# Optimization experiments

Hardware: AMD Instinct MI355X
Metric: run time of the kernel (lower is better)

## Reference

```python
import jax, jax.numpy as jnp
import numpy as np

SEQ_LEN = 1024
CHANNELS = 64
UNITS = 32
WIDTH = 64
BATCH = 4
EPS = 1e-7


def setup_inputs() -> dict:
    key = jax.random.key(0)
    ks = jax.random.split(key, 5)
    x = jax.random.normal(ks[0], (BATCH, CHANNELS, SEQ_LEN), dtype=jnp.float32)
    Wt = jax.random.normal(ks[1], (UNITS, CHANNELS), dtype=jnp.float32) * (1.0 / np.sqrt(CHANNELS))
    Wx = jax.random.normal(ks[2], (UNITS, CHANNELS), dtype=jnp.float32) * (1.0 / np.sqrt(CHANNELS))
    Wa_w = jax.random.normal(ks[3], (1, UNITS), dtype=jnp.float32) * (1.0 / np.sqrt(UNITS))
    Wa_b = jnp.zeros((1,), dtype=jnp.float32)
    bh = jnp.zeros((UNITS,), dtype=jnp.float32)
    return {"x": x, "Wt": Wt, "Wx": Wx, "Wa_w": Wa_w, "Wa_b": Wa_b, "bh": bh}


def reference(x, Wt, Wx, Wa_w, Wa_b, bh):
    # x: (B, C, S) -> xt: (B, S, C)
    xt = jnp.transpose(x, (0, 2, 1))
    q = jnp.einsum('bsc,uc->bsu', xt, Wt)          # (B, S, U)
    k = jnp.einsum('bsc,uc->bsu', xt, Wx)          # (B, S, U)
    # additive (Bahdanau) scores: tanh over broadcast sum -> (B, S, S, U)
    h = jnp.tanh(q[:, :, None, :] + k[:, None, :, :] + bh)
    e = jnp.einsum('bstu,u->bst', h, Wa_w[0]) + Wa_b[0]   # (B, S, S)
    e = jnp.exp(e - jnp.max(e, axis=-1, keepdims=True))
    # local window mask: key index t allowed for query s iff s-W//2 <= t < s-W//2+W
    idx = jnp.arange(SEQ_LEN)
    lower = idx - WIDTH // 2                        # (S,)
    mask = (lower[:, None] <= idx[None, :]) & (idx[None, :] < (lower[:, None] + WIDTH))
    e = e * mask.astype(e.dtype)
    a = e / (jnp.sum(e, axis=-1, keepdims=True) + EPS)    # (B, S, S)
    v = jnp.einsum('bst,btc->bsc', a, xt)           # (B, S, C)
    v = jnp.transpose(v, (0, 2, 1))                 # (B, C, S)
    return (v, a)
```

## Files before the change

kernel.cpp:

```cpp
#include <hip/hip_runtime.h>
#include <cstddef>
#include <cmath>

#define SEQ    1024
#define CH     64
#define UNITS  32
#define WIDTH  64
#define HALFW  32
#define BATCH  4
#define EPS    1e-7f

#define TS     8
#define TT     72
#define XS     76
#define SCS    65


__global__ __launch_bounds__(256) void qk_kernel(
    const float* __restrict__ x, const float* __restrict__ Wt,
    const float* __restrict__ Wx, const float* __restrict__ bh,
    float* __restrict__ q2, float* __restrict__ k2)
{
    int bu = blockIdx.x;
    int u  = bu & (UNITS - 1);
    int b  = bu >> 5;
    int s4 = (int)threadIdx.x << 2;

    const float* wt = Wt + u * CH;
    const float* wx = Wx + u * CH;
    const float* xb = x + (size_t)b * CH * SEQ + s4;

    float4 qa = {0.f, 0.f, 0.f, 0.f};
    float4 ka = {0.f, 0.f, 0.f, 0.f};
#pragma unroll
    for (int c = 0; c < CH; ++c) {
        float4 xv = *reinterpret_cast<const float4*>(xb + (size_t)c * SEQ);
        float wtc = wt[c], wxc = wx[c];
        qa.x = fmaf(xv.x, wtc, qa.x); qa.y = fmaf(xv.y, wtc, qa.y);
        qa.z = fmaf(xv.z, wtc, qa.z); qa.w = fmaf(xv.w, wtc, qa.w);
        ka.x = fmaf(xv.x, wxc, ka.x); ka.y = fmaf(xv.y, wxc, ka.y);
        ka.z = fmaf(xv.z, wxc, ka.z); ka.w = fmaf(xv.w, wxc, ka.w);
    }
    float bhu = bh[u];
    qa.x = 2.f * (qa.x + bhu); qa.y = 2.f * (qa.y + bhu);
    qa.z = 2.f * (qa.z + bhu); qa.w = 2.f * (qa.w + bhu);
    ka.x *= 2.f; ka.y *= 2.f; ka.z *= 2.f; ka.w *= 2.f;

    size_t o = (size_t)bu * SEQ + s4;
    *reinterpret_cast<float4*>(q2 + o) = qa;
    *reinterpret_cast<float4*>(k2 + o) = ka;
}

__global__ __launch_bounds__(256) void score_kernel(
    const float* __restrict__ q2, const float* __restrict__ k2,
    const float* __restrict__ Wa_w, float* __restrict__ aout)
{
    __shared__ float kt[UNITS * XS];
    __shared__ float qt[UNITS * TS];
    __shared__ float sc[TS * SCS];
    __shared__ float wa_s[UNITS];

    int tid = threadIdx.x;
    int blk = blockIdx.x;
    int b   = blk >> 7;
    int s0  = (blk & 127) << 3;
    int t0  = s0 - HALFW;

    const float* qb = q2 + (size_t)b * UNITS * SEQ;
    const float* kb = k2 + (size_t)b * UNITS * SEQ;

    {
        int u = tid >> 3, sl = tid & 7;
        qt[u * TS + sl] = qb[u * SEQ + s0 + sl];
    }
    if (tid < UNITS) wa_s[tid] = -2.f * Wa_w[tid];

    if (t0 >= 0 && t0 + TT <= SEQ) {
#pragma unroll
        for (int i = 0; i < 3; ++i) {
            int idx = i * 256 + tid;
            if (idx < UNITS * 18) {
                int u = idx / 18, p = idx - u * 18;
                float4 v4 = *reinterpret_cast<const float4*>(kb + u * SEQ + t0 + (p << 2));
                *reinterpret_cast<float4*>(&kt[u * XS + (p << 2)]) = v4;
            }
        }
    } else {
#pragma unroll
        for (int i = 0; i < 9; ++i) {
            int idx = i * 256 + tid;
            int u = idx / TT, tt = idx - u * TT;
            int t = t0 + tt; t = t < 0 ? 0 : (t >= SEQ ? SEQ - 1 : t);
            kt[u * XS + tt] = kb[u * SEQ + t];
        }
    }
    __syncthreads();

    {
        int sl = tid >> 5, tlg = tid & 31;
        float e0 = 0.f, e1 = 0.f;
#pragma unroll
        for (int u = 0; u < UNITS; ++u) {
            float qv = qt[u * TS + sl];
            float k0 = kt[u * XS + sl + tlg];
            float k1 = kt[u * XS + sl + tlg + 32];
            float wa = wa_s[u];
            float r0 = __builtin_amdgcn_rcpf(__expf(qv + k0) + 1.f);
            float r1 = __builtin_amdgcn_rcpf(__expf(qv + k1) + 1.f);
            e0 = fmaf(wa, r0, e0);
            e1 = fmaf(wa, r1, e1);
        }
        int ta = t0 + sl + tlg, tb = t0 + sl + tlg + 32;
        if (ta < 0 || ta >= SEQ) e0 = -INFINITY;
        if (tb < 0 || tb >= SEQ) e1 = -INFINITY;
        sc[sl * SCS + tlg]      = e0;
        sc[sl * SCS + tlg + 32] = e1;
    }
    __syncthreads();

    {
        int lane = tid & 63, wv = tid >> 6;
        int row  = wv * 2 + (lane >> 5);
        int l32  = lane & 31;
        float e0 = sc[row * SCS + l32];
        float e1 = sc[row * SCS + l32 + 32];
        float m = fmaxf(e0, e1);
#pragma unroll
        for (int off = 16; off >= 1; off >>= 1) m = fmaxf(m, __shfl_xor(m, off));
        float p0 = __expf(e0 - m), p1 = __expf(e1 - m);
        float ssum = p0 + p1;
#pragma unroll
        for (int off = 16; off >= 1; off >>= 1) ssum += __shfl_xor(ssum, off);
        float inv = __builtin_amdgcn_rcpf(ssum + EPS);
        sc[row * SCS + l32]      = p0 * inv;
        sc[row * SCS + l32 + 32] = p1 * inv;
    }
    __syncthreads();

    float* arow = aout + ((size_t)(b * SEQ + s0)) * SEQ;
    int i0 = tid << 2;
#pragma unroll
    for (int r = 0; r < TS; ++r) {
        int lowerAbs = s0 + r - HALFW;
        int d = i0 - lowerAbs;
        float4 v4 = {0.f, 0.f, 0.f, 0.f};
        if (d > -4 && d < WIDTH) {
            const float* row = sc + r * SCS;
            if (d >= 0     && d     < WIDTH) v4.x = row[d];
            if (d + 1 >= 0 && d + 1 < WIDTH) v4.y = row[d + 1];
            if (d + 2 >= 0 && d + 2 < WIDTH) v4.z = row[d + 2];
            if (d + 3 >= 0 && d + 3 < WIDTH) v4.w = row[d + 3];
        }
        *reinterpret_cast<float4*>(arow + (size_t)r * SEQ + i0) = v4;
    }
}

__global__ __launch_bounds__(256) void v_kernel(
    const float* __restrict__ x, const float* __restrict__ aout,
    float* __restrict__ out)
{
    __shared__ float xt[CH * XS];
    __shared__ float sc[TS * SCS];

    int tid = threadIdx.x;
    int blk = blockIdx.x;
    int b   = blk >> 7;
    int s0  = (blk & 127) << 3;
    int t0  = s0 - HALFW;

    const float* xb = x + (size_t)b * CH * SEQ;

    if (t0 >= 0 && t0 + TT <= SEQ) {
#pragma unroll
        for (int i = 0; i < 5; ++i) {
            int idx = i * 256 + tid;
            if (idx < CH * 18) {
                int c = idx / 18, p = idx - c * 18;
                float4 v4 = *reinterpret_cast<const float4*>(xb + c * SEQ + t0 + (p << 2));
                *reinterpret_cast<float4*>(&xt[c * XS + (p << 2)]) = v4;
            }
        }
    } else {
#pragma unroll
        for (int i = 0; i < 18; ++i) {
            int idx = i * 256 + tid;
            int c = idx / TT, tt = idx - c * TT;
            int t = t0 + tt; t = t < 0 ? 0 : (t >= SEQ ? SEQ - 1 : t);
            xt[c * XS + tt] = xb[c * SEQ + t];
        }
    }

    {
        const float* ab = aout + ((size_t)(b * SEQ + s0)) * SEQ;
#pragma unroll
        for (int i = 0; i < 2; ++i) {
            int idx = i * 256 + tid;
            int r = idx >> 6, j = idx & 63;
            int t = t0 + r + j;
            float av = (t >= 0 && t < SEQ) ? ab[(size_t)r * SEQ + t] : 0.f;
            sc[r * SCS + j] = av;
        }
    }
    __syncthreads();

    {
        int slv = tid & 7, c0 = (tid >> 3) << 1;
        float acc0 = 0.f, acc1 = 0.f;
        const float* x0 = xt + c0 * XS + slv;
        const float* x1 = x0 + XS;
        const float* ar = sc + slv * SCS;
#pragma unroll
        for (int j = 0; j < WIDTH; ++j) {
            float av = ar[j];
            acc0 = fmaf(av, x0[j], acc0);
            acc1 = fmaf(av, x1[j], acc1);
        }
        out[((size_t)(b * CH + c0)) * SEQ + s0 + slv]     = acc0;
        out[((size_t)(b * CH + c0 + 1)) * SEQ + s0 + slv] = acc1;
    }
}

extern "C" void kernel_launch(void* const* d_in, const int* in_sizes, int n_in,
                              void* d_out, int out_size, void* d_ws, size_t ws_size,
                              hipStream_t stream) {
    const float* x    = (const float*)d_in[0];
    const float* Wt   = (const float*)d_in[1];
    const float* Wx   = (const float*)d_in[2];
    const float* Wa_w = (const float*)d_in[3];
    const float* bh   = (const float*)d_in[5];
    float* out = (float*)d_out;

    float* q2   = out;
    float* k2   = out + (size_t)BATCH * UNITS * SEQ;
    float* aout = out + (size_t)BATCH * CH * SEQ;

    qk_kernel<<<BATCH * UNITS, 256, 0, stream>>>(x, Wt, Wx, bh, q2, k2);
    score_kernel<<<BATCH * (SEQ / TS), 256, 0, stream>>>(q2, k2, Wa_w, aout);
    v_kernel<<<BATCH * (SEQ / TS), 256, 0, stream>>>(x, aout, out);
}
```

Before: 83.68 us.

## Fuse score and value kernels into one attention kernel

Merges score_kernel and v_kernel into a single attn_kernel. Each block now loads its x window into shared memory alongside the k window, writes the attention row, then computes the weighted sum over x directly from the normalized scores already in shared memory. This drops one kernel launch and the global re-read of attention weights and x in a second pass. Because v output is now written while other blocks still read q2/k2, those buffers move from the output region to the workspace. The cost is higher shared-memory use per block.

```diff
diff --git a/kernel.cpp b/kernel.cpp
--- a/kernel.cpp
+++ b/kernel.cpp
@@ -51,10 +51,12 @@
     *reinterpret_cast<float4*>(k2 + o) = ka;
 }
 
-__global__ __launch_bounds__(256) void score_kernel(
+__global__ __launch_bounds__(256) void attn_kernel(
+    const float* __restrict__ x,
     const float* __restrict__ q2, const float* __restrict__ k2,
-    const float* __restrict__ Wa_w, float* __restrict__ aout)
+    const float* __restrict__ Wa_w, float* __restrict__ out)
 {
+    __shared__ float xt[CH * XS];
     __shared__ float kt[UNITS * XS];
     __shared__ float qt[UNITS * TS];
     __shared__ float sc[TS * SCS];
@@ -66,6 +68,7 @@
     int s0  = (blk & 127) << 3;
     int t0  = s0 - HALFW;
 
+    const float* xb = x  + (size_t)b * CH * SEQ;
     const float* qb = q2 + (size_t)b * UNITS * SEQ;
     const float* kb = k2 + (size_t)b * UNITS * SEQ;
 
@@ -85,6 +88,15 @@
                 *reinterpret_cast<float4*>(&kt[u * XS + (p << 2)]) = v4;
             }
         }
+#pragma unroll
+        for (int i = 0; i < 5; ++i) {
+            int idx = i * 256 + tid;
+            if (idx < CH * 18) {
+                int c = idx / 18, p = idx - c * 18;
+                float4 v4 = *reinterpret_cast<const float4*>(xb + c * SEQ + t0 + (p << 2));
+                *reinterpret_cast<float4*>(&xt[c * XS + (p << 2)]) = v4;
+            }
+        }
     } else {
 #pragma unroll
         for (int i = 0; i < 9; ++i) {
@@ -92,6 +104,13 @@
             int u = idx / TT, tt = idx - u * TT;
             int t = t0 + tt; t = t < 0 ? 0 : (t >= SEQ ? SEQ - 1 : t);
             kt[u * XS + tt] = kb[u * SEQ + t];
+        }
+#pragma unroll
+        for (int i = 0; i < 18; ++i) {
+            int idx = i * 256 + tid;
+            int c = idx / TT, tt = idx - c * TT;
+            int t = t0 + tt; t = t < 0 ? 0 : (t >= SEQ ? SEQ - 1 : t);
+            xt[c * XS + tt] = xb[c * SEQ + t];
         }
     }
     __syncthreads();
@@ -137,7 +156,7 @@
     }
     __syncthreads();
 
-    float* arow = aout + ((size_t)(b * SEQ + s0)) * SEQ;
+    float* arow = out + (size_t)BATCH * CH * SEQ + ((size_t)(b * SEQ + s0)) * SEQ;
     int i0 = tid << 2;
 #pragma unroll
     for (int r = 0; r < TS; ++r) {
@@ -153,55 +172,6 @@
         }
         *reinterpret_cast<float4*>(arow + (size_t)r * SEQ + i0) = v4;
     }
-}
-
-__global__ __launch_bounds__(256) void v_kernel(
-    const float* __restrict__ x, const float* __restrict__ aout,
-    float* __restrict__ out)
-{
-    __shared__ float xt[CH * XS];
-    __shared__ float sc[TS * SCS];
-
-    int tid = threadIdx.x;
-    int blk = blockIdx.x;
-    int b   = blk >> 7;
-    int s0  = (blk & 127) << 3;
-    int t0  = s0 - HALFW;
-
-    const float* xb = x + (size_t)b * CH * SEQ;
-
-    if (t0 >= 0 && t0 + TT <= SEQ) {
-#pragma unroll
-        for (int i = 0; i < 5; ++i) {
-            int idx = i * 256 + tid;
-            if (idx < CH * 18) {
-                int c = idx / 18, p = idx - c * 18;
-                float4 v4 = *reinterpret_cast<const float4*>(xb + c * SEQ + t0 + (p << 2));
-                *reinterpret_cast<float4*>(&xt[c * XS + (p << 2)]) = v4;
-            }
-        }
-    } else {
-#pragma unroll
-        for (int i = 0; i < 18; ++i) {
-            int idx = i * 256 + tid;
-            int c = idx / TT, tt = idx - c * TT;
-            int t = t0 + tt; t = t < 0 ? 0 : (t >= SEQ ? SEQ - 1 : t);
-            xt[c * XS + tt] = xb[c * SEQ + t];
-        }
-    }
-
-    {
-        const float* ab = aout + ((size_t)(b * SEQ + s0)) * SEQ;
-#pragma unroll
-        for (int i = 0; i < 2; ++i) {
-            int idx = i * 256 + tid;
-            int r = idx >> 6, j = idx & 63;
-            int t = t0 + r + j;
-            float av = (t >= 0 && t < SEQ) ? ab[(size_t)r * SEQ + t] : 0.f;
-            sc[r * SCS + j] = av;
-        }
-    }
-    __syncthreads();
 
     {
         int slv = tid & 7, c0 = (tid >> 3) << 1;
@@ -230,11 +200,9 @@
     const float* bh   = (const float*)d_in[5];
     float* out = (float*)d_out;
 
-    float* q2   = out;
-    float* k2   = out + (size_t)BATCH * UNITS * SEQ;
-    float* aout = out + (size_t)BATCH * CH * SEQ;
+    float* q2 = (float*)d_ws;
+    float* k2 = q2 + (size_t)BATCH * UNITS * SEQ;
 
     qk_kernel<<<BATCH * UNITS, 256, 0, stream>>>(x, Wt, Wx, bh, q2, k2);
-    score_kernel<<<BATCH * (SEQ / TS), 256, 0, stream>>>(q2, k2, Wa_w, aout);
-    v_kernel<<<BATCH * (SEQ / TS), 256, 0, stream>>>(x, aout, out);
+    attn_kernel<<<BATCH * (SEQ / TS), 256, 0, stream>>>(x, q2, k2, Wa_w, out);
 }
```

Result: faster. 79.21 us (-5.3%).
